# Optimization experiments

Hardware: AMD Instinct MI355X
Metric: run time of the kernel (lower is better)

Reference implementation:

```python
import jax, jax.numpy as jnp
import numpy as np

TEMPERATURE = 8.0  # sqrt(d_k)
WINDOW = 2
GATE_THRESH = 0.5
NEG_INF = -1e30


def setup_inputs() -> dict:
    key = jax.random.key(0)
    k1, k2, k3, k4 = jax.random.split(key, 4)
    BH, L, D = 32, 2048, 64
    return {
        "q": jax.random.normal(k1, (BH, L, D), dtype=jnp.float32),
        "k": jax.random.normal(k2, (BH, L, D), dtype=jnp.float32),
        "v": jax.random.normal(k3, (BH, L, D), dtype=jnp.float32),
        "gate_w": jax.random.normal(k4, (1, D), dtype=jnp.float32) * 0.1,
        "gate_b": jnp.zeros((1,), dtype=jnp.float32),
    }


def reference(q, k, v, gate_w, gate_b):
    # q,k: [BH, L, D]; v: [BH, L, Dv]
    BH, Lq, D = q.shape
    Lk = k.shape[1]
    attn = jnp.einsum("bqd,bkd->bqk", q, k) / TEMPERATURE  # [BH, Lq, Lk]
    # per-query gate: if sigmoid(linear(q)) <= thresh, restrict to sliding window
    gate = jax.nn.sigmoid(jnp.einsum("bqd,od->bqo", q, gate_w) + gate_b) > GATE_THRESH  # [BH,Lq,1]
    i = jnp.arange(Lq)[:, None]
    j = jnp.arange(Lk)[None, :]
    window_ok = jnp.abs(i - j) <= WINDOW  # [Lq, Lk]; equals left=max(0,i-W), right=min(Lk,i+W+1)
    allowed = gate | window_ok[None, :, :]  # gate True -> full attention
    attn = jnp.where(allowed, attn, NEG_INF)
    attn = jax.nn.softmax(attn, axis=2)
    # dropout omitted (eval mode)
    out = jnp.einsum("bqk,bkd->bqd", attn, v)
    return out, attn
```

## Files before the change

kernel.cpp:

```cpp
#include <hip/hip_runtime.h>


typedef short bf16x8 __attribute__((ext_vector_type(8)));
typedef float f32x4  __attribute__((ext_vector_type(4)));

#define LSEQ 2048
#define DDIM 64
#define KB_STRIDE 72
#define VT_STRIDE 36
#define PB_STRIDE 36

__device__ __forceinline__ unsigned short f2bf(float x) {
    unsigned int u = __float_as_uint(x);
    u += 0x7FFFu + ((u >> 16) & 1u);
    return (unsigned short)(u >> 16);
}

__global__ __launch_bounds__(256)
void dsa_attn_kernel(const float* __restrict__ Q,
                     const float* __restrict__ K,
                     const float* __restrict__ V,
                     const float* __restrict__ GW,
                     const float* __restrict__ GB,
                     float* __restrict__ OUT,
                     float* __restrict__ ATT)
{
    __shared__ unsigned short Kbuf[32 * KB_STRIDE];
    __shared__ unsigned short Vt[64 * VT_STRIDE];
    __shared__ float Pbuf[4][16 * PB_STRIDE];
    __shared__ float gateF[64];

    const int bx   = blockIdx.x;
    const int bh   = bx >> 5;
    const int q0   = (bx & 31) << 6;
    const int tid  = threadIdx.x;
    const int wave = tid >> 6;
    const int lane = tid & 63;
    const int m16  = lane & 15;
    const int quad = lane >> 4;

    const float* qb = Q + ((size_t)bh * LSEQ + q0) * DDIM;
    const float* kb = K + (size_t)bh * LSEQ * DDIM;
    const float* vb = V + (size_t)bh * LSEQ * DDIM;

    if (tid < 64) {
        const float* qr = qb + tid * DDIM;
        float a = 0.f;
        #pragma unroll 8
        for (int d = 0; d < DDIM; ++d) a += qr[d] * GW[d];
        a += GB[0];
        gateF[tid] = (a > 0.f) ? 1.f : 0.f;
    }

    bf16x8 qfrag[2];
    {
        const float* qr = qb + ((wave << 4) + m16) * DDIM + (quad << 3);
        #pragma unroll
        for (int db = 0; db < 2; ++db) {
            const float* p = qr + db * 32;
            bf16x8 f;
            #pragma unroll
            for (int j = 0; j < 8; ++j) f[j] = (short)f2bf(p[j]);
            qfrag[db] = f;
        }
    }

    __syncthreads();
    float gate[4];
    int   irow[4];
    #pragma unroll
    for (int r = 0; r < 4; ++r) {
        gate[r] = gateF[(wave << 4) + (quad << 2) + r];
        irow[r] = q0 + (wave << 4) + (quad << 2) + r;
    }

    float lsum[4] = {0.f, 0.f, 0.f, 0.f};
    for (int kt = 0; kt < LSEQ / 32; ++kt) {
        __syncthreads();
        {
            const int e   = tid << 3;
            const int key = e >> 6;
            const int d   = e & 63;
            const float* src = kb + (size_t)(kt * 32 + key) * DDIM + d;
            unsigned short* dst = &Kbuf[key * KB_STRIDE + d];
            #pragma unroll
            for (int j = 0; j < 8; ++j) dst[j] = f2bf(src[j]);
        }
        __syncthreads();
        #pragma unroll
        for (int nt = 0; nt < 2; ++nt) {
            const unsigned short* kr = &Kbuf[(nt * 16 + m16) * KB_STRIDE + (quad << 3)];
            bf16x8 kf0 = *(const bf16x8*)(kr);
            bf16x8 kf1 = *(const bf16x8*)(kr + 32);
            f32x4 acc = {0.f, 0.f, 0.f, 0.f};
            acc = __builtin_amdgcn_mfma_f32_16x16x32_bf16(qfrag[0], kf0, acc, 0, 0, 0);
            acc = __builtin_amdgcn_mfma_f32_16x16x32_bf16(qfrag[1], kf1, acc, 0, 0, 0);
            const int jcol = kt * 32 + nt * 16 + m16;
            #pragma unroll
            for (int r = 0; r < 4; ++r) {
                int dist = irow[r] - jcol; if (dist < 0) dist = -dist;
                const bool allowed = (gate[r] > 0.5f) || (dist <= 2);
                const float s = acc[r] * 0.125f;
                lsum[r] += allowed ? __expf(s) : 0.f;
            }
        }
    }
    #pragma unroll
    for (int r = 0; r < 4; ++r) {
        float x = lsum[r];
        x += __shfl_xor(x, 1);
        x += __shfl_xor(x, 2);
        x += __shfl_xor(x, 4);
        x += __shfl_xor(x, 8);
        lsum[r] = 1.0f / x;
    }

    f32x4 oacc[4];
    #pragma unroll
    for (int dt = 0; dt < 4; ++dt) oacc[dt] = (f32x4){0.f, 0.f, 0.f, 0.f};

    for (int kt = 0; kt < LSEQ / 32; ++kt) {
        __syncthreads();
        {
            const int e   = tid << 3;
            const int key = e >> 6;
            const int d   = e & 63;
            const float* src = kb + (size_t)(kt * 32 + key) * DDIM + d;
            unsigned short* dst = &Kbuf[key * KB_STRIDE + d];
            #pragma unroll
            for (int j = 0; j < 8; ++j) dst[j] = f2bf(src[j]);
        }
        {
            const int key = tid & 31;
            const int db  = (tid >> 5) << 3;
            const float* src = vb + (size_t)(kt * 32 + key) * DDIM + db;
            #pragma unroll
            for (int j = 0; j < 8; ++j)
                Vt[(db + j) * VT_STRIDE + key] = f2bf(src[j]);
        }
        __syncthreads();

        #pragma unroll
        for (int nt = 0; nt < 2; ++nt) {
            const unsigned short* kr = &Kbuf[(nt * 16 + m16) * KB_STRIDE + (quad << 3)];
            bf16x8 kf0 = *(const bf16x8*)(kr);
            bf16x8 kf1 = *(const bf16x8*)(kr + 32);
            f32x4 acc = {0.f, 0.f, 0.f, 0.f};
            acc = __builtin_amdgcn_mfma_f32_16x16x32_bf16(qfrag[0], kf0, acc, 0, 0, 0);
            acc = __builtin_amdgcn_mfma_f32_16x16x32_bf16(qfrag[1], kf1, acc, 0, 0, 0);
            const int jcol = kt * 32 + nt * 16 + m16;
            #pragma unroll
            for (int r = 0; r < 4; ++r) {
                int dist = irow[r] - jcol; if (dist < 0) dist = -dist;
                const bool allowed = (gate[r] > 0.5f) || (dist <= 2);
                const float s = acc[r] * 0.125f;
                const float p = allowed ? __expf(s) * lsum[r] : 0.f;
                Pbuf[wave][((quad << 2) + r) * PB_STRIDE + nt * 16 + m16] = p;
            }
        }
        __syncthreads();

        const float* pr = &Pbuf[wave][m16 * PB_STRIDE + (quad << 3)];
        f32x4 p0 = *(const f32x4*)(pr);
        f32x4 p1 = *(const f32x4*)(pr + 4);
        float* ap = ATT + ((size_t)bh * LSEQ + q0 + (wave << 4) + m16) * LSEQ
                        + kt * 32 + (quad << 3);
        *(f32x4*)(ap)     = p0;
        *(f32x4*)(ap + 4) = p1;

        bf16x8 pf;
        #pragma unroll
        for (int j = 0; j < 4; ++j) {
            pf[j]     = (short)f2bf(p0[j]);
            pf[4 + j] = (short)f2bf(p1[j]);
        }
        #pragma unroll
        for (int dt = 0; dt < 4; ++dt) {
            const unsigned short* vr = &Vt[(dt * 16 + m16) * VT_STRIDE + (quad << 3)];
            ushort4 va  = *(const ushort4*)(vr);
            ushort4 vb4 = *(const ushort4*)(vr + 4);
            bf16x8 vf;
            vf[0] = (short)va.x;  vf[1] = (short)va.y;
            vf[2] = (short)va.z;  vf[3] = (short)va.w;
            vf[4] = (short)vb4.x; vf[5] = (short)vb4.y;
            vf[6] = (short)vb4.z; vf[7] = (short)vb4.w;
            oacc[dt] = __builtin_amdgcn_mfma_f32_16x16x32_bf16(pf, vf, oacc[dt], 0, 0, 0);
        }
    }

    float* ob = OUT + ((size_t)bh * LSEQ + q0 + (wave << 4)) * DDIM;
    #pragma unroll
    for (int dt = 0; dt < 4; ++dt) {
        #pragma unroll
        for (int r = 0; r < 4; ++r) {
            ob[((quad << 2) + r) * DDIM + dt * 16 + m16] = oacc[dt][r];
        }
    }
}

extern "C" void kernel_launch(void* const* d_in, const int* in_sizes, int n_in,
                              void* d_out, int out_size, void* d_ws, size_t ws_size,
                              hipStream_t stream) {
    const float* q  = (const float*)d_in[0];
    const float* k  = (const float*)d_in[1];
    const float* v  = (const float*)d_in[2];
    const float* gw = (const float*)d_in[3];
    const float* gb = (const float*)d_in[4];

    float* out  = (float*)d_out;
    float* attn = out + (size_t)32 * 2048 * 64;

    dim3 grid(32 * (2048 / 64));
    dim3 block(256);
    dsa_attn_kernel<<<grid, block, 0, stream>>>(q, k, v, gw, gb, out, attn);
}
```

Measured before the change: 792.2 us.

## Precompute bf16 K and transposed V in workspace, drop LDS staging and barriers

Adds two pre-pass kernels that convert K to bf16 and V to a transposed bf16 layout in the workspace. The attention kernel then loads MFMA fragments straight from global memory instead of staging them through LDS, which removes the per-tile block barriers and the redundant per-block fp32-to-bf16 conversion. It also computes the gate per wave with shuffles, uses per-wave P buffers without block syncs, and writes the attention matrix with nontemporal stores. In exchange it adds extra kernel launches and workspace traffic, and it relies on global/L2 hits for K and V reuse across the 32 query blocks of each head.

```diff
diff --git a/kernel.cpp b/kernel.cpp
--- a/kernel.cpp
+++ b/kernel.cpp
@@ -4,10 +4,9 @@
 typedef short bf16x8 __attribute__((ext_vector_type(8)));
 typedef float f32x4  __attribute__((ext_vector_type(4)));
 
+#define BH   32
 #define LSEQ 2048
 #define DDIM 64
-#define KB_STRIDE 72
-#define VT_STRIDE 36
 #define PB_STRIDE 36
 
 __device__ __forceinline__ unsigned short f2bf(float x) {
@@ -17,18 +16,60 @@
 }
 
 __global__ __launch_bounds__(256)
+void conv_k_kernel(const float* __restrict__ K, unsigned short* __restrict__ Kb)
+{
+    const size_t i = ((size_t)blockIdx.x * 256 + threadIdx.x) * 8;
+    f32x4 a = *(const f32x4*)(K + i);
+    f32x4 b = *(const f32x4*)(K + i + 4);
+    ushort4 lo, hi;
+    lo.x = f2bf(a[0]); lo.y = f2bf(a[1]); lo.z = f2bf(a[2]); lo.w = f2bf(a[3]);
+    hi.x = f2bf(b[0]); hi.y = f2bf(b[1]); hi.z = f2bf(b[2]); hi.w = f2bf(b[3]);
+    *(ushort4*)(Kb + i)     = lo;
+    *(ushort4*)(Kb + i + 4) = hi;
+}
+
+__global__ __launch_bounds__(256)
+void conv_vt_kernel(const float* __restrict__ V, unsigned short* __restrict__ Vt)
+{
+    __shared__ float tile[64][65];
+    const int bh   = blockIdx.x >> 5;
+    const int key0 = (blockIdx.x & 31) << 6;
+    const int tid  = threadIdx.x;
+
+    const float* src = V + ((size_t)bh * LSEQ + key0) * DDIM;
+    #pragma unroll
+    for (int i = 0; i < 4; ++i) {
+        const int f   = tid + 256 * i;
+        const int row = f >> 4;
+        const int c4  = f & 15;
+        f32x4 x = *(const f32x4*)(src + row * DDIM + c4 * 4);
+        tile[row][c4 * 4 + 0] = x[0];
+        tile[row][c4 * 4 + 1] = x[1];
+        tile[row][c4 * 4 + 2] = x[2];
+        tile[row][c4 * 4 + 3] = x[3];
+    }
+    __syncthreads();
+    const int d    = tid >> 2;
+    const int kseg = (tid & 3) << 4;
+    unsigned short* dst = Vt + ((size_t)bh * DDIM + d) * LSEQ + key0 + kseg;
+    ushort4 o[4];
+    #pragma unroll
+    for (int j = 0; j < 16; ++j)
+        ((unsigned short*)o)[j] = f2bf(tile[kseg + j][d]);
+    #pragma unroll
+    for (int j = 0; j < 4; ++j) *(ushort4*)(dst + j * 4) = o[j];
+}
+
+__global__ __launch_bounds__(256)
 void dsa_attn_kernel(const float* __restrict__ Q,
-                     const float* __restrict__ K,
-                     const float* __restrict__ V,
+                     const unsigned short* __restrict__ Kb,
+                     const unsigned short* __restrict__ Vt,
                      const float* __restrict__ GW,
                      const float* __restrict__ GB,
                      float* __restrict__ OUT,
                      float* __restrict__ ATT)
 {
-    __shared__ unsigned short Kbuf[32 * KB_STRIDE];
-    __shared__ unsigned short Vt[64 * VT_STRIDE];
     __shared__ float Pbuf[4][16 * PB_STRIDE];
-    __shared__ float gateF[64];
 
     const int bx   = blockIdx.x;
     const int bh   = bx >> 5;
@@ -38,73 +79,61 @@
     const int lane = tid & 63;
     const int m16  = lane & 15;
     const int quad = lane >> 4;
-
-    const float* qb = Q + ((size_t)bh * LSEQ + q0) * DDIM;
-    const float* kb = K + (size_t)bh * LSEQ * DDIM;
-    const float* vb = V + (size_t)bh * LSEQ * DDIM;
-
-    if (tid < 64) {
-        const float* qr = qb + tid * DDIM;
-        float a = 0.f;
-        #pragma unroll 8
-        for (int d = 0; d < DDIM; ++d) a += qr[d] * GW[d];
-        a += GB[0];
-        gateF[tid] = (a > 0.f) ? 1.f : 0.f;
-    }
+    const int qw   = q0 + (wave << 4);
+
+    const float* qr = Q + ((size_t)bh * LSEQ + qw + m16) * DDIM;
+    const unsigned short* kbh = Kb + (size_t)bh * LSEQ * DDIM;
+    const unsigned short* vbh = Vt + (size_t)bh * DDIM * LSEQ;
 
     bf16x8 qfrag[2];
+    #pragma unroll
+    for (int db = 0; db < 2; ++db) {
+        const float* p = qr + db * 32 + (quad << 3);
+        bf16x8 f;
+        #pragma unroll
+        for (int j = 0; j < 8; ++j) f[j] = (short)f2bf(p[j]);
+        qfrag[db] = f;
+    }
+    float g = 0.f;
     {
-        const float* qr = qb + ((wave << 4) + m16) * DDIM + (quad << 3);
-        #pragma unroll
-        for (int db = 0; db < 2; ++db) {
-            const float* p = qr + db * 32;
-            bf16x8 f;
-            #pragma unroll
-            for (int j = 0; j < 8; ++j) f[j] = (short)f2bf(p[j]);
-            qfrag[db] = f;
-        }
-    }
-
-    __syncthreads();
-    float gate[4];
+        const float* p = qr + (quad << 4);
+        #pragma unroll
+        for (int j = 0; j < 16; ++j) g += p[j] * GW[(quad << 4) + j];
+        g += __shfl_xor(g, 16);
+        g += __shfl_xor(g, 32);
+        g += GB[0];
+    }
+    bool  gate[4];
     int   irow[4];
     #pragma unroll
     for (int r = 0; r < 4; ++r) {
-        gate[r] = gateF[(wave << 4) + (quad << 2) + r];
-        irow[r] = q0 + (wave << 4) + (quad << 2) + r;
+        const int row = (quad << 2) + r;
+        gate[r] = __shfl(g, row) > 0.f;
+        irow[r] = qw + row;
     }
 
     float lsum[4] = {0.f, 0.f, 0.f, 0.f};
+    #pragma unroll 2
     for (int kt = 0; kt < LSEQ / 32; ++kt) {
-        __syncthreads();
-        {
-            const int e   = tid << 3;
-            const int key = e >> 6;
-            const int d   = e & 63;
-            const float* src = kb + (size_t)(kt * 32 + key) * DDIM + d;
-            unsigned short* dst = &Kbuf[key * KB_STRIDE + d];
-            #pragma unroll
-            for (int j = 0; j < 8; ++j) dst[j] = f2bf(src[j]);
-        }
-        __syncthreads();
         #pragma unroll
         for (int nt = 0; nt < 2; ++nt) {
-            const unsigned short* kr = &Kbuf[(nt * 16 + m16) * KB_STRIDE + (quad << 3)];
-            bf16x8 kf0 = *(const bf16x8*)(kr);
-            bf16x8 kf1 = *(const bf16x8*)(kr + 32);
+            const int keyb = kt * 32 + nt * 16;
+            const unsigned short* kp = kbh + (size_t)(keyb + m16) * DDIM + (quad << 3);
+            bf16x8 kf0 = *(const bf16x8*)(kp);
+            bf16x8 kf1 = *(const bf16x8*)(kp + 32);
             f32x4 acc = {0.f, 0.f, 0.f, 0.f};
             acc = __builtin_amdgcn_mfma_f32_16x16x32_bf16(qfrag[0], kf0, acc, 0, 0, 0);
             acc = __builtin_amdgcn_mfma_f32_16x16x32_bf16(qfrag[1], kf1, acc, 0, 0, 0);
-            const int jcol = kt * 32 + nt * 16 + m16;
+            const int jcol = keyb + m16;
             #pragma unroll
             for (int r = 0; r < 4; ++r) {
                 int dist = irow[r] - jcol; if (dist < 0) dist = -dist;
-                const bool allowed = (gate[r] > 0.5f) || (dist <= 2);
-                const float s = acc[r] * 0.125f;
-                lsum[r] += allowed ? __expf(s) : 0.f;
+                const bool allowed = gate[r] || (dist <= 2);
+                lsum[r] += allowed ? __expf(acc[r] * 0.125f) : 0.f;
             }
         }
     }
+    float linv[4];
     #pragma unroll
     for (int r = 0; r < 4; ++r) {
         float x = lsum[r];
@@ -112,61 +141,41 @@
         x += __shfl_xor(x, 2);
         x += __shfl_xor(x, 4);
         x += __shfl_xor(x, 8);
-        lsum[r] = 1.0f / x;
+        linv[r] = 1.0f / x;
     }
 
     f32x4 oacc[4];
     #pragma unroll
     for (int dt = 0; dt < 4; ++dt) oacc[dt] = (f32x4){0.f, 0.f, 0.f, 0.f};
 
+    float* prow = &Pbuf[wave][0];
+    #pragma unroll 2
     for (int kt = 0; kt < LSEQ / 32; ++kt) {
-        __syncthreads();
-        {
-            const int e   = tid << 3;
-            const int key = e >> 6;
-            const int d   = e & 63;
-            const float* src = kb + (size_t)(kt * 32 + key) * DDIM + d;
-            unsigned short* dst = &Kbuf[key * KB_STRIDE + d];
-            #pragma unroll
-            for (int j = 0; j < 8; ++j) dst[j] = f2bf(src[j]);
-        }
-        {
-            const int key = tid & 31;
-            const int db  = (tid >> 5) << 3;
-            const float* src = vb + (size_t)(kt * 32 + key) * DDIM + db;
-            #pragma unroll
-            for (int j = 0; j < 8; ++j)
-                Vt[(db + j) * VT_STRIDE + key] = f2bf(src[j]);
-        }
-        __syncthreads();
-
         #pragma unroll
         for (int nt = 0; nt < 2; ++nt) {
-            const unsigned short* kr = &Kbuf[(nt * 16 + m16) * KB_STRIDE + (quad << 3)];
-            bf16x8 kf0 = *(const bf16x8*)(kr);
-            bf16x8 kf1 = *(const bf16x8*)(kr + 32);
+            const int keyb = kt * 32 + nt * 16;
+            const unsigned short* kp = kbh + (size_t)(keyb + m16) * DDIM + (quad << 3);
+            bf16x8 kf0 = *(const bf16x8*)(kp);
+            bf16x8 kf1 = *(const bf16x8*)(kp + 32);
             f32x4 acc = {0.f, 0.f, 0.f, 0.f};
             acc = __builtin_amdgcn_mfma_f32_16x16x32_bf16(qfrag[0], kf0, acc, 0, 0, 0);
             acc = __builtin_amdgcn_mfma_f32_16x16x32_bf16(qfrag[1], kf1, acc, 0, 0, 0);
-            const int jcol = kt * 32 + nt * 16 + m16;
+            const int jcol = keyb + m16;
             #pragma unroll
             for (int r = 0; r < 4; ++r) {
                 int dist = irow[r] - jcol; if (dist < 0) dist = -dist;
-                const bool allowed = (gate[r] > 0.5f) || (dist <= 2);
-                const float s = acc[r] * 0.125f;
-                const float p = allowed ? __expf(s) * lsum[r] : 0.f;
-                Pbuf[wave][((quad << 2) + r) * PB_STRIDE + nt * 16 + m16] = p;
+                const bool allowed = gate[r] || (dist <= 2);
+                const float p = allowed ? __expf(acc[r] * 0.125f) * linv[r] : 0.f;
+                prow[(((quad << 2) + r) * PB_STRIDE) + nt * 16 + m16] = p;
             }
         }
-        __syncthreads();
-
-        const float* pr = &Pbuf[wave][m16 * PB_STRIDE + (quad << 3)];
+        const float* pr = prow + m16 * PB_STRIDE + (quad << 3);
         f32x4 p0 = *(const f32x4*)(pr);
         f32x4 p1 = *(const f32x4*)(pr + 4);
-        float* ap = ATT + ((size_t)bh * LSEQ + q0 + (wave << 4) + m16) * LSEQ
-                        + kt * 32 + (quad << 3);
-        *(f32x4*)(ap)     = p0;
-        *(f32x4*)(ap + 4) = p1;
+
+        float* ap = ATT + ((size_t)bh * LSEQ + qw + m16) * LSEQ + kt * 32 + (quad << 3);
+        __builtin_nontemporal_store(p0, (f32x4*)(ap));
+        __builtin_nontemporal_store(p1, (f32x4*)(ap + 4));
 
         bf16x8 pf;
         #pragma unroll
@@ -176,19 +185,13 @@
         }
         #pragma unroll
         for (int dt = 0; dt < 4; ++dt) {
-            const unsigned short* vr = &Vt[(dt * 16 + m16) * VT_STRIDE + (quad << 3)];
-            ushort4 va  = *(const ushort4*)(vr);
-            ushort4 vb4 = *(const ushort4*)(vr + 4);
-            bf16x8 vf;
-            vf[0] = (short)va.x;  vf[1] = (short)va.y;
-            vf[2] = (short)va.z;  vf[3] = (short)va.w;
-            vf[4] = (short)vb4.x; vf[5] = (short)vb4.y;
-            vf[6] = (short)vb4.z; vf[7] = (short)vb4.w;
+            const unsigned short* vp = vbh + (size_t)(dt * 16 + m16) * LSEQ + kt * 32 + (quad << 3);
+            bf16x8 vf = *(const bf16x8*)(vp);
             oacc[dt] = __builtin_amdgcn_mfma_f32_16x16x32_bf16(pf, vf, oacc[dt], 0, 0, 0);
         }
     }
 
-    float* ob = OUT + ((size_t)bh * LSEQ + q0 + (wave << 4)) * DDIM;
+    float* ob = OUT + ((size_t)bh * LSEQ + qw) * DDIM;
     #pragma unroll
     for (int dt = 0; dt < 4; ++dt) {
         #pragma unroll
@@ -208,9 +211,15 @@
     const float* gb = (const float*)d_in[4];
 
     float* out  = (float*)d_out;
-    float* attn = out + (size_t)32 * 2048 * 64;
-
-    dim3 grid(32 * (2048 / 64));
-    dim3 block(256);
-    dsa_attn_kernel<<<grid, block, 0, stream>>>(q, k, v, gw, gb, out, attn);
-}
+    float* attn = out + (size_t)BH * LSEQ * DDIM;
+
+    unsigned short* Kb = (unsigned short*)d_ws;
+    unsigned short* Vt = Kb + (size_t)BH * LSEQ * DDIM;
+
+    const size_t nelem = (size_t)BH * LSEQ * DDIM;
+    conv_k_kernel <<<dim3(nelem / (256 * 8)), dim3(256), 0, stream>>>(k, Kb);
+    conv_vt_kernel<<<dim3(BH * (LSEQ / 64)),  dim3(256), 0, stream>>>(v, Vt);
+
+    dsa_attn_kernel<<<dim3(BH * (LSEQ / 64)), dim3(256), 0, stream>>>(
+        q, Kb, Vt, gw, gb, out, attn);
+}
```

Result: slower. 860.1 us (+8.6%).
